# Kernel tuning notes

Hardware: AMD Instinct MI355X
Metric: run time of the kernel (lower is better)

The kernel has to match this reference:

```python
import jax, jax.numpy as jnp
import numpy as np

NUM_GROUPS = 8
EPS = 1e-5


def setup_inputs() -> dict:
    key = jax.random.key(0)
    ks = jax.random.split(key, 10)
    b, c, h, w = 4, 64, 64, 64
    x = jax.random.normal(ks[0], (b, c, h, w), dtype=jnp.float32)
    # GroupNorm affine params (default init: weight=1, bias=0; randomize slightly for testing)
    gamma = jnp.ones((c,), jnp.float32) + 0.01 * jax.random.normal(ks[1], (c,))
    beta = 0.01 * jax.random.normal(ks[2], (c,))
    # 1x1 conv weights as [out_c, in_c] matrices (xavier-uniform), biases zeros in torch init
    def xavier(k, shape):
        fan = shape[0] + shape[1]
        lim = jnp.sqrt(6.0 / fan)
        return jax.random.uniform(k, shape, jnp.float32, -lim, lim)
    Wq = xavier(ks[3], (c, c)); bq = jnp.zeros((c,), jnp.float32)
    Wk = xavier(ks[4], (c, c)); bk = jnp.zeros((c,), jnp.float32)
    Wv = xavier(ks[5], (c, c)); bv = jnp.zeros((c,), jnp.float32)
    Wp = xavier(ks[6], (c, c)); bp = jnp.zeros((c,), jnp.float32)
    return {"x": x, "gamma": gamma, "beta": beta,
            "Wq": Wq, "bq": bq, "Wk": Wk, "bk": bk,
            "Wv": Wv, "bv": bv, "Wp": Wp, "bp": bp}


def group_norm(x, gamma, beta):
    b, c, h, w = x.shape
    g = NUM_GROUPS
    xg = x.reshape(b, g, c // g, h, w)
    mean = jnp.mean(xg, axis=(2, 3, 4), keepdims=True)
    var = jnp.var(xg, axis=(2, 3, 4), keepdims=True)
    xn = ((xg - mean) * jax.lax.rsqrt(var + EPS)).reshape(b, c, h, w)
    return xn * gamma[None, :, None, None] + beta[None, :, None, None]


def reference(x, gamma, beta, Wq, bq, Wk, bk, Wv, bv, Wp, bp):
    b, c, h, w = x.shape
    n = h * w
    xn = group_norm(x, gamma, beta)
    xn_flat = xn.reshape(b, c, n)  # [b, c, n]
    # 1x1 convs == channel-wise linear maps
    q = jnp.einsum('oc,bcn->bno', Wq, xn_flat) + bq  # [b, n, c]
    k = jnp.einsum('oc,bcn->bon', Wk, xn_flat) + bk[None, :, None]  # [b, c, n]
    v = jnp.einsum('oc,bcn->bno', Wv, xn_flat) + bv  # [b, n, c]
    attn = jax.nn.softmax(jnp.einsum('bnc,bcm->bnm', q, k) / jnp.sqrt(jnp.float32(c)), axis=-1)
    out = jnp.einsum('bnm,bmc->bnc', attn, v)  # [b, n, c]
    out = out.transpose(0, 2, 1).reshape(b, c, h, w)
    out = jnp.einsum('oc,bchw->bohw', Wp, out) + bp[None, :, None, None]
    return out + x
```

## Files before the change

kernel.cpp:

```cpp
#include <hip/hip_runtime.h>
#include <hip/hip_bf16.h>
#include <math.h>

#define BATCH 4
#define CH    64
#define NPOS  4096
#define NGRP  8
#define CPG   8
#define GEPS  1e-5f
#define NSPLIT 8
#define LOG2E 1.4426950408889634f

typedef __attribute__((ext_vector_type(8))) short bf16x8;
typedef __attribute__((ext_vector_type(4))) float f32x4;

__device__ __forceinline__ ushort f2bf(float f) {
    union { float f; uint32_t u; } v; v.f = f;
    uint32_t r = v.u + 0x7fffu + ((v.u >> 16) & 1u);
    return (ushort)(r >> 16);
}
__device__ __forceinline__ float bf2f(ushort u) {
    union { uint32_t u; float f; } v; v.u = ((uint32_t)u) << 16; return v.f;
}

__device__ __forceinline__ uint32_t swz(uint32_t row, uint32_t byteInRow) {
    return (row << 7) + (byteInRow ^ ((row & 7u) << 4));
}

__device__ __forceinline__ bf16x8 ldfrag(const ushort* base, int row, int kbyte) {
    return *(const bf16x8*)((const char*)base + swz(row, kbyte));
}

__global__ __launch_bounds__(256) void gn_part_kernel(const float* __restrict__ x,
                                                      float2* __restrict__ part) {
    const int blk = blockIdx.x;
    const float4* xp4 = (const float4*)(x + (size_t)blk * 4096);
    float s1 = 0.f, s2 = 0.f;
    for (int i = threadIdx.x; i < 1024; i += 256) {
        float4 t = xp4[i];
        s1 += t.x + t.y + t.z + t.w;
        s2 += t.x * t.x + t.y * t.y + t.z * t.z + t.w * t.w;
    }
    __shared__ float sh1[256], sh2[256];
    const int tid = threadIdx.x;
    sh1[tid] = s1; sh2[tid] = s2;
    __syncthreads();
    for (int off = 128; off > 0; off >>= 1) {
        if (tid < off) { sh1[tid] += sh1[tid + off]; sh2[tid] += sh2[tid + off]; }
        __syncthreads();
    }
    if (tid == 0) { float2 r; r.x = sh1[0]; r.y = sh2[0]; part[blk] = r; }
}

__global__ __launch_bounds__(256) void qkv_mfma_kernel(
    const float* __restrict__ x, const float2* __restrict__ part,
    const float* __restrict__ gamma, const float* __restrict__ beta,
    const float* __restrict__ Wq, const float* __restrict__ bq,
    const float* __restrict__ Wk, const float* __restrict__ bk,
    const float* __restrict__ Wv, const float* __restrict__ bv,
    ushort* __restrict__ qg, ushort* __restrict__ kg, ushort* __restrict__ vg)
{
    __shared__ ushort xn[64 * 64];
    __shared__ ushort Wl[64 * 64];
    __shared__ ushort ob[64 * 64];
    __shared__ float st[16];

    const int tid = threadIdx.x;
    const int w = tid >> 6, lane = tid & 63, g = lane >> 4, q16 = lane & 15;
    const int m = blockIdx.x >> 8;
    const int bidx = blockIdx.x & 255;
    const int b = bidx >> 6, n0 = (bidx & 63) << 6;

    const float* W = (m == 0) ? Wq : (m == 1) ? Wk : Wv;

    {
        const int row = tid >> 2, cb = (tid & 3) << 4;
#pragma unroll
        for (int j = 0; j < 4; ++j) {
            float4 v = *(const float4*)(W + row * 64 + cb + j * 4);
            ushort4 h; h.x = f2bf(v.x); h.y = f2bf(v.y); h.z = f2bf(v.z); h.w = f2bf(v.w);
            *(ushort4*)((char*)Wl + swz(row, (cb + j * 4) * 2)) = h;
        }
    }
    if (tid < 64) {
        float2 p = part[b * 64 + tid];
        float s1 = p.x, s2 = p.y;
        s1 += __shfl_xor(s1, 1); s2 += __shfl_xor(s2, 1);
        s1 += __shfl_xor(s1, 2); s2 += __shfl_xor(s2, 2);
        s1 += __shfl_xor(s1, 4); s2 += __shfl_xor(s2, 4);
        if ((tid & 7) == 0) {
            const float inv = 1.0f / (float)(CPG * NPOS);
            float mean = s1 * inv;
            float var  = s2 * inv - mean * mean;
            st[(tid >> 3) * 2]     = mean;
            st[(tid >> 3) * 2 + 1] = rsqrtf(var + GEPS);
        }
    }
    __syncthreads();

    {
        const int c = tid >> 2, nb = (tid & 3) << 4;
        const float mean = st[(c >> 3) * 2];
        const float rstd = st[(c >> 3) * 2 + 1];
        const float gmm = gamma[c] * rstd;
        const float btt = beta[c] - mean * gmm;
        const float* xp = x + (((size_t)(b * CH + c)) << 12) + n0 + nb;
#pragma unroll
        for (int j = 0; j < 4; ++j) {
            float4 v = *(const float4*)(xp + j * 4);
            float vv[4] = {v.x, v.y, v.z, v.w};
#pragma unroll
            for (int e = 0; e < 4; ++e) {
                int n = nb + j * 4 + e;
                *(ushort*)((char*)xn + swz(n, c * 2)) = f2bf(vv[e] * gmm + btt);
            }
        }
    }
    __syncthreads();

    if (m < 2) {
        const float* bias = m ? bk : bq;
        const float scl = m ? 1.0f : 0.125f * LOG2E;
        bf16x8 ax0 = ldfrag(xn, (w << 4) + q16, (g << 4));
        bf16x8 ax1 = ldfrag(xn, (w << 4) + q16, 64 + (g << 4));
#pragma unroll
        for (int ot = 0; ot < 4; ++ot) {
            f32x4 acc = {0.f, 0.f, 0.f, 0.f};
            bf16x8 b0 = ldfrag(Wl, (ot << 4) + q16, (g << 4));
            bf16x8 b1 = ldfrag(Wl, (ot << 4) + q16, 64 + (g << 4));
            acc = __builtin_amdgcn_mfma_f32_16x16x32_bf16(ax0, b0, acc, 0, 0, 0);
            acc = __builtin_amdgcn_mfma_f32_16x16x32_bf16(ax1, b1, acc, 0, 0, 0);
            float bs = bias[(ot << 4) + q16];
#pragma unroll
            for (int r = 0; r < 4; ++r)
                *(ushort*)((char*)ob + swz((w << 4) + (g << 2) + r, ((ot << 4) + q16) << 1)) =
                    f2bf((acc[r] + bs) * scl);
        }
        __syncthreads();
        ushort* dst = (m ? kg : qg) + (((size_t)b) << 18);
#pragma unroll
        for (int i = 0; i < 2; ++i) {
            const int G = tid + (i << 8);
            const int lane_ = G & 63;
            const int h = (G >> 6) & 1;
            const int colb = (h << 5) + ((lane_ >> 4) << 3);
            if (m == 0) {
                const int qgi = (G >> 7) & 1;
                const int qgl = G >> 8;
                const int row = (qgl << 5) + (qgi << 4) + (lane_ & 15);
                int4 d = *(const int4*)((char*)ob + swz(row, colb << 1));
                *(int4*)(dst + (((size_t)(n0 >> 5) + qgl) << 11)
                             + ((size_t)((((qgi << 1) + h) << 6) + lane_) << 3)) = d;
            } else {
                const int nt = G >> 7;
                const int row = (nt << 4) + (lane_ & 15);
                int4 d = *(const int4*)((char*)ob + swz(row, colb << 1));
                *(int4*)(dst + ((size_t)(n0 >> 6) << 12)
                             + ((size_t)((((nt << 1) + h) << 6) + lane_) << 3)) = d;
            }
        }
    } else {
        bf16x8 aw0 = ldfrag(Wl, (w << 4) + q16, (g << 4));
        bf16x8 aw1 = ldfrag(Wl, (w << 4) + q16, 64 + (g << 4));
#pragma unroll
        for (int nt = 0; nt < 4; ++nt) {
            f32x4 acc = {0.f, 0.f, 0.f, 0.f};
            bf16x8 b0 = ldfrag(xn, (nt << 4) + q16, (g << 4));
            bf16x8 b1 = ldfrag(xn, (nt << 4) + q16, 64 + (g << 4));
            acc = __builtin_amdgcn_mfma_f32_16x16x32_bf16(aw0, b0, acc, 0, 0, 0);
            acc = __builtin_amdgcn_mfma_f32_16x16x32_bf16(aw1, b1, acc, 0, 0, 0);
#pragma unroll
            for (int r = 0; r < 4; ++r) {
                float bs = bv[(w << 4) + (g << 2) + r];
                *(ushort*)((char*)ob + swz((w << 4) + (g << 2) + r, ((nt << 4) + q16) << 1)) =
                    f2bf(acc[r] + bs);
            }
        }
        __syncthreads();
        ushort* dst = vg + (((size_t)b) << 18) + ((size_t)(n0 >> 6) << 12);
#pragma unroll
        for (int i = 0; i < 2; ++i) {
            const int G = tid + (i << 8);
            const int lane_ = G & 63;
            const int h = (G >> 6) & 1;
            const int ct = G >> 7;
            const int row = (ct << 4) + (lane_ & 15);
            const int colb = (h << 5) + ((lane_ >> 4) << 3);
            int4 d = *(const int4*)((char*)ob + swz(row, colb << 1));
            *(int4*)(dst + ((size_t)((((ct << 1) + h) << 6) + lane_) << 3)) = d;
        }
    }
}

#define LOADK(KF, KT)                                                          \
    _Pragma("unroll") for (int nt = 0; nt < 4; ++nt)                           \
    _Pragma("unroll") for (int h = 0; h < 2; ++h)                              \
        KF[nt][h] = *(const bf16x8*)(kp + (((size_t)(KT)) << 12) +             \
                     ((size_t)((((nt << 1) + h) << 6) + lane) << 3));

#define STEP(KF, KFN, KT, PREF)                                                \
  do {                                                                         \
    bf16x8 vf[4][2];                                                           \
    _Pragma("unroll") for (int ct = 0; ct < 4; ++ct)                           \
    _Pragma("unroll") for (int h = 0; h < 2; ++h)                              \
        vf[ct][h] = *(const bf16x8*)(vp + (((size_t)(KT)) << 12) +             \
                     ((size_t)((((ct << 1) + h) << 6) + lane) << 3));          \
    if (PREF) { LOADK(KFN, (KT) + 1); }                                        \
    f32x4 s_[4][2];                                                            \
    _Pragma("unroll") for (int nt = 0; nt < 4; ++nt)                           \
    _Pragma("unroll") for (int qgi = 0; qgi < 2; ++qgi) {                      \
        f32x4 z = {0.f, 0.f, 0.f, 0.f};                                        \
        z = __builtin_amdgcn_mfma_f32_16x16x32_bf16(KF[nt][0], aq[qgi][0], z, 0, 0, 0); \
        z = __builtin_amdgcn_mfma_f32_16x16x32_bf16(KF[nt][1], aq[qgi][1], z, 0, 0, 0); \
        s_[nt][qgi] = z;                                                       \
    }                                                                          \
    _Pragma("unroll") for (int qgi = 0; qgi < 2; ++qgi) {                      \
        float rs = 0.0f;                                                       \
        _Pragma("unroll") for (int nt = 0; nt < 4; ++nt) {                     \
            float p0 = exp2f(s_[nt][qgi][0]);                                  \
            float p1 = exp2f(s_[nt][qgi][1]);                                  \
            float p2 = exp2f(s_[nt][qgi][2]);                                  \
            float p3 = exp2f(s_[nt][qgi][3]);                                  \
            rs += (p0 + p1) + (p2 + p3);                                       \
            float2 t01; t01.x = p0; t01.y = p1;                                \
            float2 t23; t23.x = p2; t23.y = p3;                                \
            __hip_bfloat162 b01 = __float22bfloat162_rn(t01);                  \
            __hip_bfloat162 b23 = __float22bfloat162_rn(t23);                  \
            uint2 pk; pk.x = *(uint32_t*)&b01; pk.y = *(uint32_t*)&b23;        \
            *(uint2*)((char*)Pw + swz((qgi << 4) + q16, (nt << 5) + (lg << 3))) = pk; \
        }                                                                      \
        rs += __shfl_xor(rs, 16);                                              \
        rs += __shfl_xor(rs, 32);                                              \
        l_[qgi] += rs;                                                         \
    }                                                                          \
    asm volatile("" ::: "memory");                                             \
    bf16x8 pb[2][2];                                                           \
    _Pragma("unroll") for (int qgi = 0; qgi < 2; ++qgi) {                      \
        pb[qgi][0] = ldfrag(Pw, (qgi << 4) + q16, (lg << 4));                  \
        pb[qgi][1] = ldfrag(Pw, (qgi << 4) + q16, 64 + (lg << 4));             \
    }                                                                          \
    _Pragma("unroll") for (int ct = 0; ct < 4; ++ct)                           \
    _Pragma("unroll") for (int qgi = 0; qgi < 2; ++qgi) {                      \
        f32x4 o = o_[ct][qgi];                                                 \
        o = __builtin_amdgcn_mfma_f32_16x16x32_bf16(vf[ct][0], pb[qgi][0], o, 0, 0, 0); \
        o = __builtin_amdgcn_mfma_f32_16x16x32_bf16(vf[ct][1], pb[qgi][1], o, 0, 0, 0); \
        o_[ct][qgi] = o;                                                       \
    }                                                                          \
  } while (0)

__global__ __launch_bounds__(256) void attn_mfma_kernel(
    const ushort* __restrict__ qg, const ushort* __restrict__ kg,
    const ushort* __restrict__ vg,
    ushort* __restrict__ opart, float* __restrict__ lpart)
{
    __shared__ ushort Ps[4][32 * 64];

    const int tid = threadIdx.x;
    const int w = tid >> 6, lane = tid & 63, lg = lane >> 4, q16 = lane & 15;
    const int logical = ((blockIdx.x & 7) << 7) + (blockIdx.x >> 3);
    const int ks = logical & 7;
    const int qb = (logical >> 3) & 31;
    const int b  = logical >> 8;
    const int q0 = (qb << 7) + (w << 5);
    const ushort* qp = qg + (((size_t)b) << 18) + ((size_t)((qb << 2) + w) << 11);
    const ushort* kp = kg + (((size_t)b) << 18) + ((size_t)ks << 15);
    const ushort* vp = vg + (((size_t)b) << 18) + ((size_t)ks << 15);
    ushort* Pw = Ps[w];

    bf16x8 aq[2][2];
#pragma unroll
    for (int qgi = 0; qgi < 2; ++qgi)
#pragma unroll
        for (int h = 0; h < 2; ++h)
            aq[qgi][h] = *(const bf16x8*)(qp + ((size_t)((((qgi << 1) + h) << 6) + lane) << 3));

    float l_[2] = {0.f, 0.f};
    f32x4 o_[4][2];
#pragma unroll
    for (int ct = 0; ct < 4; ++ct)
#pragma unroll
        for (int qgi = 0; qgi < 2; ++qgi) o_[ct][qgi] = (f32x4){0.f, 0.f, 0.f, 0.f};

    bf16x8 kfA[4][2], kfB[4][2];
    LOADK(kfA, 0);

#pragma unroll 1
    for (int kt2 = 0; kt2 < 8; kt2 += 2) {
        STEP(kfA, kfB, kt2, true);
        STEP(kfB, kfA, kt2 + 1, (kt2 + 1) < 7);
    }

    const size_t bs = (size_t)(b * NSPLIT + ks);
#pragma unroll
    for (int qgi = 0; qgi < 2; ++qgi) {
        const int n = q0 + (qgi << 4) + q16;
        ushort* ob = opart + ((bs * 64) << 12) + n;
#pragma unroll
        for (int ct = 0; ct < 4; ++ct)
#pragma unroll
            for (int r = 0; r < 4; ++r)
                ob[((size_t)((ct << 4) + (lg << 2) + r)) << 12] = f2bf(o_[ct][qgi][r]);
    }
    if (lg == 0) {
#pragma unroll
        for (int qgi = 0; qgi < 2; ++qgi) {
            const int n = q0 + (qgi << 4) + q16;
            lpart[bs * 4096 + n] = l_[qgi];
        }
    }
}

__global__ __launch_bounds__(256) void combine_kernel(
    const ushort* __restrict__ opart, const float* __restrict__ lpart,
    const float* __restrict__ x, const float* __restrict__ Wp,
    const float* __restrict__ bp, float* __restrict__ out)
{
    __shared__ ushort Obf[64 * 64];
    __shared__ ushort Wps[64 * 64];
    __shared__ float as_[64];

    const int tid = threadIdx.x;
    const int w = tid >> 6, lane = tid & 63, g = lane >> 4, q16 = lane & 15;
    const int b = blockIdx.x >> 6, n0 = (blockIdx.x & 63) << 6;

    {
        const int row = tid >> 2, cb = (tid & 3) << 4;
#pragma unroll
        for (int j = 0; j < 4; ++j) {
            float4 v = *(const float4*)(Wp + row * 64 + cb + j * 4);
            ushort4 h; h.x = f2bf(v.x); h.y = f2bf(v.y); h.z = f2bf(v.z); h.w = f2bf(v.w);
            *(ushort4*)((char*)Wps + swz(row, (cb + j * 4) * 2)) = h;
        }
    }
    if (tid < 64) {
        const int n = n0 + tid;
        float d = 0.f;
#pragma unroll
        for (int s = 0; s < NSPLIT; ++s)
            d += lpart[(size_t)(b * NSPLIT + s) * 4096 + n];
        as_[tid] = 1.0f / d;
    }
    __syncthreads();

    {
        const int c = tid >> 2, nb = (tid & 3) << 4;
        const ushort* base = opart + ((((size_t)(b * NSPLIT)) * 64 + c) << 12) + n0 + nb;
        const size_t sstride = (size_t)64 << 12;
        float acc[16];
#pragma unroll
        for (int e = 0; e < 16; ++e) acc[e] = 0.f;
#pragma unroll
        for (int s = 0; s < NSPLIT; ++s) {
            const ushort* p = base + s * sstride;
            uint4 d0 = *(const uint4*)(p);
            uint4 d1 = *(const uint4*)(p + 8);
            const uint uw[8] = {d0.x, d0.y, d0.z, d0.w, d1.x, d1.y, d1.z, d1.w};
#pragma unroll
            for (int j = 0; j < 8; ++j) {
                acc[2 * j]     += bf2f((ushort)(uw[j] & 0xffffu));
                acc[2 * j + 1] += bf2f((ushort)(uw[j] >> 16));
            }
        }
#pragma unroll
        for (int e = 0; e < 16; ++e) {
            int nl = nb + e;
            *(ushort*)((char*)Obf + swz(nl, c << 1)) = f2bf(acc[e] * as_[nl]);
        }
    }
    __syncthreads();

    {
        bf16x8 aw0 = ldfrag(Wps, (w << 4) + q16, (g << 4));
        bf16x8 aw1 = ldfrag(Wps, (w << 4) + q16, 64 + (g << 4));
        float bpv[4];
#pragma unroll
        for (int r = 0; r < 4; ++r) bpv[r] = bp[(w << 4) + (g << 2) + r];
#pragma unroll
        for (int qt = 0; qt < 4; ++qt) {
            f32x4 d = {0.f, 0.f, 0.f, 0.f};
            bf16x8 b0 = ldfrag(Obf, (qt << 4) + q16, (g << 4));
            bf16x8 b1 = ldfrag(Obf, (qt << 4) + q16, 64 + (g << 4));
            d = __builtin_amdgcn_mfma_f32_16x16x32_bf16(aw0, b0, d, 0, 0, 0);
            d = __builtin_amdgcn_mfma_f32_16x16x32_bf16(aw1, b1, d, 0, 0, 0);
#pragma unroll
            for (int r = 0; r < 4; ++r) {
                int oc = (w << 4) + (g << 2) + r;
                size_t addr = (((size_t)(b * CH + oc)) << 12) + n0 + (qt << 4) + q16;
                out[addr] = d[r] + bpv[r] + x[addr];
            }
        }
    }
}

extern "C" void kernel_launch(void* const* d_in, const int* in_sizes, int n_in,
                              void* d_out, int out_size, void* d_ws, size_t ws_size,
                              hipStream_t stream) {
    const float* x     = (const float*)d_in[0];
    const float* gamma = (const float*)d_in[1];
    const float* beta  = (const float*)d_in[2];
    const float* Wq    = (const float*)d_in[3];
    const float* bq    = (const float*)d_in[4];
    const float* Wk    = (const float*)d_in[5];
    const float* bk    = (const float*)d_in[6];
    const float* Wv    = (const float*)d_in[7];
    const float* bv    = (const float*)d_in[8];
    const float* Wp    = (const float*)d_in[9];
    const float* bp    = (const float*)d_in[10];
    float* out = (float*)d_out;

    float2* part = (float2*)d_ws;
    ushort* q_t = (ushort*)((char*)d_ws + 4096);
    ushort* k_t = q_t + (size_t)BATCH * NPOS * CH;
    ushort* v_t = k_t + (size_t)BATCH * NPOS * CH;
    ushort* opart = (ushort*)((char*)d_ws + 4096 + (size_t)3 * BATCH * NPOS * CH * 2);
    float* lpart = (float*)((char*)opart + (size_t)BATCH * NSPLIT * CH * NPOS * 2);

    hipLaunchKernelGGL(gn_part_kernel, dim3(256), dim3(256), 0, stream, x, part);
    hipLaunchKernelGGL(qkv_mfma_kernel, dim3(768), dim3(256), 0, stream,
                       x, part, gamma, beta, Wq, bq, Wk, bk, Wv, bv, q_t, k_t, v_t);
    hipLaunchKernelGGL(attn_mfma_kernel, dim3(1024), dim3(256), 0, stream,
                       q_t, k_t, v_t, opart, lpart);
    hipLaunchKernelGGL(combine_kernel, dim3(BATCH * 64), dim3(256), 0, stream,
                       opart, lpart, x, Wp, bp, out);
}
```

Baseline: 53.68 us.

## Process 64 queries per wave in attention kernel to reuse K/V fragments

Each wave in the attention kernel now handles 64 query rows instead of 32, so each K and V tile loaded from global memory feeds twice as many MFMAs. The grid shrinks from 1024 to 512 blocks and the shared P scratch doubles. The explicit double-buffered K prefetch macro is dropped in favour of loading K per n-tile inside the loop. This cuts K/V global traffic per query, at the cost of more registers (accumulators double), lower occupancy, fewer blocks for 256 CUs, and less latency hiding for K loads.

Result: slower. 63.46 us (+18.2%).

```diff
diff --git a/kernel.cpp b/kernel.cpp
--- a/kernel.cpp
+++ b/kernel.cpp
@@ -192,107 +192,110 @@
     }
 }
 
-#define LOADK(KF, KT)                                                          \
-    _Pragma("unroll") for (int nt = 0; nt < 4; ++nt)                           \
-    _Pragma("unroll") for (int h = 0; h < 2; ++h)                              \
-        KF[nt][h] = *(const bf16x8*)(kp + (((size_t)(KT)) << 12) +             \
-                     ((size_t)((((nt << 1) + h) << 6) + lane) << 3));
-
-#define STEP(KF, KFN, KT, PREF)                                                \
-  do {                                                                         \
-    bf16x8 vf[4][2];                                                           \
-    _Pragma("unroll") for (int ct = 0; ct < 4; ++ct)                           \
-    _Pragma("unroll") for (int h = 0; h < 2; ++h)                              \
-        vf[ct][h] = *(const bf16x8*)(vp + (((size_t)(KT)) << 12) +             \
-                     ((size_t)((((ct << 1) + h) << 6) + lane) << 3));          \
-    if (PREF) { LOADK(KFN, (KT) + 1); }                                        \
-    f32x4 s_[4][2];                                                            \
-    _Pragma("unroll") for (int nt = 0; nt < 4; ++nt)                           \
-    _Pragma("unroll") for (int qgi = 0; qgi < 2; ++qgi) {                      \
-        f32x4 z = {0.f, 0.f, 0.f, 0.f};                                        \
-        z = __builtin_amdgcn_mfma_f32_16x16x32_bf16(KF[nt][0], aq[qgi][0], z, 0, 0, 0); \
-        z = __builtin_amdgcn_mfma_f32_16x16x32_bf16(KF[nt][1], aq[qgi][1], z, 0, 0, 0); \
-        s_[nt][qgi] = z;                                                       \
-    }                                                                          \
-    _Pragma("unroll") for (int qgi = 0; qgi < 2; ++qgi) {                      \
-        float rs = 0.0f;                                                       \
-        _Pragma("unroll") for (int nt = 0; nt < 4; ++nt) {                     \
-            float p0 = exp2f(s_[nt][qgi][0]);                                  \
-            float p1 = exp2f(s_[nt][qgi][1]);                                  \
-            float p2 = exp2f(s_[nt][qgi][2]);                                  \
-            float p3 = exp2f(s_[nt][qgi][3]);                                  \
-            rs += (p0 + p1) + (p2 + p3);                                       \
-            float2 t01; t01.x = p0; t01.y = p1;                                \
-            float2 t23; t23.x = p2; t23.y = p3;                                \
-            __hip_bfloat162 b01 = __float22bfloat162_rn(t01);                  \
-            __hip_bfloat162 b23 = __float22bfloat162_rn(t23);                  \
-            uint2 pk; pk.x = *(uint32_t*)&b01; pk.y = *(uint32_t*)&b23;        \
-            *(uint2*)((char*)Pw + swz((qgi << 4) + q16, (nt << 5) + (lg << 3))) = pk; \
-        }                                                                      \
-        rs += __shfl_xor(rs, 16);                                              \
-        rs += __shfl_xor(rs, 32);                                              \
-        l_[qgi] += rs;                                                         \
-    }                                                                          \
-    asm volatile("" ::: "memory");                                             \
-    bf16x8 pb[2][2];                                                           \
-    _Pragma("unroll") for (int qgi = 0; qgi < 2; ++qgi) {                      \
-        pb[qgi][0] = ldfrag(Pw, (qgi << 4) + q16, (lg << 4));                  \
-        pb[qgi][1] = ldfrag(Pw, (qgi << 4) + q16, 64 + (lg << 4));             \
-    }                                                                          \
-    _Pragma("unroll") for (int ct = 0; ct < 4; ++ct)                           \
-    _Pragma("unroll") for (int qgi = 0; qgi < 2; ++qgi) {                      \
-        f32x4 o = o_[ct][qgi];                                                 \
-        o = __builtin_amdgcn_mfma_f32_16x16x32_bf16(vf[ct][0], pb[qgi][0], o, 0, 0, 0); \
-        o = __builtin_amdgcn_mfma_f32_16x16x32_bf16(vf[ct][1], pb[qgi][1], o, 0, 0, 0); \
-        o_[ct][qgi] = o;                                                       \
-    }                                                                          \
-  } while (0)
-
 __global__ __launch_bounds__(256) void attn_mfma_kernel(
     const ushort* __restrict__ qg, const ushort* __restrict__ kg,
     const ushort* __restrict__ vg,
     ushort* __restrict__ opart, float* __restrict__ lpart)
 {
-    __shared__ ushort Ps[4][32 * 64];
+    __shared__ ushort Ps[4][64 * 64];
 
     const int tid = threadIdx.x;
     const int w = tid >> 6, lane = tid & 63, lg = lane >> 4, q16 = lane & 15;
-    const int logical = ((blockIdx.x & 7) << 7) + (blockIdx.x >> 3);
+    const int logical = ((blockIdx.x & 7) << 6) + (blockIdx.x >> 3);
     const int ks = logical & 7;
-    const int qb = (logical >> 3) & 31;
-    const int b  = logical >> 8;
-    const int q0 = (qb << 7) + (w << 5);
-    const ushort* qp = qg + (((size_t)b) << 18) + ((size_t)((qb << 2) + w) << 11);
+    const int qb = (logical >> 3) & 15;
+    const int b  = logical >> 7;
+    const int q0 = (qb << 8) + (w << 6);
+    const int qw64 = (qb << 2) + w;
+
+    const ushort* qp = qg + (((size_t)b) << 18);
     const ushort* kp = kg + (((size_t)b) << 18) + ((size_t)ks << 15);
     const ushort* vp = vg + (((size_t)b) << 18) + ((size_t)ks << 15);
     ushort* Pw = Ps[w];
 
-    bf16x8 aq[2][2];
-#pragma unroll
-    for (int qgi = 0; qgi < 2; ++qgi)
+    bf16x8 aq[4][2];
+#pragma unroll
+    for (int qgi = 0; qgi < 4; ++qgi)
 #pragma unroll
         for (int h = 0; h < 2; ++h)
-            aq[qgi][h] = *(const bf16x8*)(qp + ((size_t)((((qgi << 1) + h) << 6) + lane) << 3));
-
-    float l_[2] = {0.f, 0.f};
-    f32x4 o_[4][2];
+            aq[qgi][h] = *(const bf16x8*)(qp
+                + ((size_t)((qw64 << 1) + (qgi >> 1)) << 11)
+                + ((size_t)(((((qgi & 1) << 1) + h) << 6) + lane) << 3));
+
+    float l_[4] = {0.f, 0.f, 0.f, 0.f};
+    f32x4 o_[4][4];
 #pragma unroll
     for (int ct = 0; ct < 4; ++ct)
 #pragma unroll
-        for (int qgi = 0; qgi < 2; ++qgi) o_[ct][qgi] = (f32x4){0.f, 0.f, 0.f, 0.f};
-
-    bf16x8 kfA[4][2], kfB[4][2];
-    LOADK(kfA, 0);
+        for (int qgi = 0; qgi < 4; ++qgi) o_[ct][qgi] = (f32x4){0.f, 0.f, 0.f, 0.f};
 
 #pragma unroll 1
-    for (int kt2 = 0; kt2 < 8; kt2 += 2) {
-        STEP(kfA, kfB, kt2, true);
-        STEP(kfB, kfA, kt2 + 1, (kt2 + 1) < 7);
+    for (int kt = 0; kt < 8; ++kt) {
+        bf16x8 vf[4][2];
+#pragma unroll
+        for (int ct = 0; ct < 4; ++ct)
+#pragma unroll
+            for (int h = 0; h < 2; ++h)
+                vf[ct][h] = *(const bf16x8*)(vp + (((size_t)kt) << 12) +
+                             ((size_t)((((ct << 1) + h) << 6) + lane) << 3));
+        float rs[4] = {0.f, 0.f, 0.f, 0.f};
+#pragma unroll
+        for (int nt = 0; nt < 4; ++nt) {
+            bf16x8 k0 = *(const bf16x8*)(kp + (((size_t)kt) << 12) +
+                         ((size_t)(((nt << 1) << 6) + lane) << 3));
+            bf16x8 k1 = *(const bf16x8*)(kp + (((size_t)kt) << 12) +
+                         ((size_t)((((nt << 1) + 1) << 6) + lane) << 3));
+            f32x4 s[4];
+#pragma unroll
+            for (int qgi = 0; qgi < 4; ++qgi) {
+                f32x4 z = {0.f, 0.f, 0.f, 0.f};
+                z = __builtin_amdgcn_mfma_f32_16x16x32_bf16(k0, aq[qgi][0], z, 0, 0, 0);
+                z = __builtin_amdgcn_mfma_f32_16x16x32_bf16(k1, aq[qgi][1], z, 0, 0, 0);
+                s[qgi] = z;
+            }
+#pragma unroll
+            for (int qgi = 0; qgi < 4; ++qgi) {
+                float p0 = exp2f(s[qgi][0]);
+                float p1 = exp2f(s[qgi][1]);
+                float p2 = exp2f(s[qgi][2]);
+                float p3 = exp2f(s[qgi][3]);
+                rs[qgi] += (p0 + p1) + (p2 + p3);
+                float2 t01; t01.x = p0; t01.y = p1;
+                float2 t23; t23.x = p2; t23.y = p3;
+                __hip_bfloat162 b01 = __float22bfloat162_rn(t01);
+                __hip_bfloat162 b23 = __float22bfloat162_rn(t23);
+                uint2 pk; pk.x = *(uint32_t*)&b01; pk.y = *(uint32_t*)&b23;
+                *(uint2*)((char*)Pw + swz((qgi << 4) + q16, (nt << 5) + (lg << 3))) = pk;
+            }
+        }
+#pragma unroll
+        for (int qgi = 0; qgi < 4; ++qgi) {
+            float r = rs[qgi];
+            r += __shfl_xor(r, 16);
+            r += __shfl_xor(r, 32);
+            l_[qgi] += r;
+        }
+        asm volatile("" ::: "memory");
+        bf16x8 pb[4][2];
+#pragma unroll
+        for (int qgi = 0; qgi < 4; ++qgi) {
+            pb[qgi][0] = ldfrag(Pw, (qgi << 4) + q16, (lg << 4));
+            pb[qgi][1] = ldfrag(Pw, (qgi << 4) + q16, 64 + (lg << 4));
+        }
+#pragma unroll
+        for (int ct = 0; ct < 4; ++ct)
+#pragma unroll
+            for (int qgi = 0; qgi < 4; ++qgi) {
+                f32x4 o = o_[ct][qgi];
+                o = __builtin_amdgcn_mfma_f32_16x16x32_bf16(vf[ct][0], pb[qgi][0], o, 0, 0, 0);
+                o = __builtin_amdgcn_mfma_f32_16x16x32_bf16(vf[ct][1], pb[qgi][1], o, 0, 0, 0);
+                o_[ct][qgi] = o;
+            }
     }
 
     const size_t bs = (size_t)(b * NSPLIT + ks);
 #pragma unroll
-    for (int qgi = 0; qgi < 2; ++qgi) {
+    for (int qgi = 0; qgi < 4; ++qgi) {
         const int n = q0 + (qgi << 4) + q16;
         ushort* ob = opart + ((bs * 64) << 12) + n;
 #pragma unroll
@@ -303,7 +306,7 @@
     }
     if (lg == 0) {
 #pragma unroll
-        for (int qgi = 0; qgi < 2; ++qgi) {
+        for (int qgi = 0; qgi < 4; ++qgi) {
             const int n = q0 + (qgi << 4) + q16;
             lpart[bs * 4096 + n] = l_[qgi];
         }
@@ -418,7 +421,7 @@
     hipLaunchKernelGGL(gn_part_kernel, dim3(256), dim3(256), 0, stream, x, part);
     hipLaunchKernelGGL(qkv_mfma_kernel, dim3(768), dim3(256), 0, stream,
                        x, part, gamma, beta, Wq, bq, Wk, bk, Wv, bv, q_t, k_t, v_t);
-    hipLaunchKernelGGL(attn_mfma_kernel, dim3(1024), dim3(256), 0, stream,
+    hipLaunchKernelGGL(attn_mfma_kernel, dim3(512), dim3(256), 0, stream,
                        q_t, k_t, v_t, opart, lpart);
     hipLaunchKernelGGL(combine_kernel, dim3(BATCH * 64), dim3(256), 0, stream,
                        opart, lpart, x, Wp, bp, out);
```

## Software-pipeline attention: overlap QK^T/exp of next tile with PV of current

Applied to the files above, without the earlier changes.

Splits the per-tile step into a score/exp block and a PV block, then double-buffers the P tile in shared memory so the scores of tile t+1 are computed before the PV MMA of tile t. The row-sum shuffles move out of the loop and run once at the end. It also adds a launch-bounds occupancy hint of 4 blocks. The aim is to hide exp and LDS latency behind MFMA work, at the cost of twice the shared memory per wave and higher register pressure.

New measurement: 76.07 us. +41.7%, slower.

```diff
diff --git a/kernel.cpp b/kernel.cpp
--- a/kernel.cpp
+++ b/kernel.cpp
@@ -198,14 +198,8 @@
         KF[nt][h] = *(const bf16x8*)(kp + (((size_t)(KT)) << 12) +             \
                      ((size_t)((((nt << 1) + h) << 6) + lane) << 3));
 
-#define STEP(KF, KFN, KT, PREF)                                                \
+#define SBLOCK(KF, PA)                                                         \
   do {                                                                         \
-    bf16x8 vf[4][2];                                                           \
-    _Pragma("unroll") for (int ct = 0; ct < 4; ++ct)                           \
-    _Pragma("unroll") for (int h = 0; h < 2; ++h)                              \
-        vf[ct][h] = *(const bf16x8*)(vp + (((size_t)(KT)) << 12) +             \
-                     ((size_t)((((ct << 1) + h) << 6) + lane) << 3));          \
-    if (PREF) { LOADK(KFN, (KT) + 1); }                                        \
     f32x4 s_[4][2];                                                            \
     _Pragma("unroll") for (int nt = 0; nt < 4; ++nt)                           \
     _Pragma("unroll") for (int qgi = 0; qgi < 2; ++qgi) {                      \
@@ -215,29 +209,33 @@
         s_[nt][qgi] = z;                                                       \
     }                                                                          \
     _Pragma("unroll") for (int qgi = 0; qgi < 2; ++qgi) {                      \
-        float rs = 0.0f;                                                       \
         _Pragma("unroll") for (int nt = 0; nt < 4; ++nt) {                     \
             float p0 = exp2f(s_[nt][qgi][0]);                                  \
             float p1 = exp2f(s_[nt][qgi][1]);                                  \
             float p2 = exp2f(s_[nt][qgi][2]);                                  \
             float p3 = exp2f(s_[nt][qgi][3]);                                  \
-            rs += (p0 + p1) + (p2 + p3);                                       \
+            l_[qgi] += (p0 + p1) + (p2 + p3);                                  \
             float2 t01; t01.x = p0; t01.y = p1;                                \
             float2 t23; t23.x = p2; t23.y = p3;                                \
             __hip_bfloat162 b01 = __float22bfloat162_rn(t01);                  \
             __hip_bfloat162 b23 = __float22bfloat162_rn(t23);                  \
             uint2 pk; pk.x = *(uint32_t*)&b01; pk.y = *(uint32_t*)&b23;        \
-            *(uint2*)((char*)Pw + swz((qgi << 4) + q16, (nt << 5) + (lg << 3))) = pk; \
+            *(uint2*)((char*)(PA) + swz((qgi << 4) + q16, (nt << 5) + (lg << 3))) = pk; \
         }                                                                      \
-        rs += __shfl_xor(rs, 16);                                              \
-        rs += __shfl_xor(rs, 32);                                              \
-        l_[qgi] += rs;                                                         \
     }                                                                          \
-    asm volatile("" ::: "memory");                                             \
+  } while (0)
+
+#define PVBLOCK(PA, KT)                                                        \
+  do {                                                                         \
+    bf16x8 vf[4][2];                                                           \
+    _Pragma("unroll") for (int ct = 0; ct < 4; ++ct)                           \
+    _Pragma("unroll") for (int h = 0; h < 2; ++h)                              \
+        vf[ct][h] = *(const bf16x8*)(vp + (((size_t)(KT)) << 12) +             \
+                     ((size_t)((((ct << 1) + h) << 6) + lane) << 3));          \
     bf16x8 pb[2][2];                                                           \
     _Pragma("unroll") for (int qgi = 0; qgi < 2; ++qgi) {                      \
-        pb[qgi][0] = ldfrag(Pw, (qgi << 4) + q16, (lg << 4));                  \
-        pb[qgi][1] = ldfrag(Pw, (qgi << 4) + q16, 64 + (lg << 4));             \
+        pb[qgi][0] = ldfrag((PA), (qgi << 4) + q16, (lg << 4));                \
+        pb[qgi][1] = ldfrag((PA), (qgi << 4) + q16, 64 + (lg << 4));           \
     }                                                                          \
     _Pragma("unroll") for (int ct = 0; ct < 4; ++ct)                           \
     _Pragma("unroll") for (int qgi = 0; qgi < 2; ++qgi) {                      \
@@ -248,12 +246,12 @@
     }                                                                          \
   } while (0)
 
-__global__ __launch_bounds__(256) void attn_mfma_kernel(
+__global__ __launch_bounds__(256, 4) void attn_mfma_kernel(
     const ushort* __restrict__ qg, const ushort* __restrict__ kg,
     const ushort* __restrict__ vg,
     ushort* __restrict__ opart, float* __restrict__ lpart)
 {
-    __shared__ ushort Ps[4][32 * 64];
+    __shared__ ushort Ps[4][2][32 * 64];
 
     const int tid = threadIdx.x;
     const int w = tid >> 6, lane = tid & 63, lg = lane >> 4, q16 = lane & 15;
@@ -265,7 +263,8 @@
     const ushort* qp = qg + (((size_t)b) << 18) + ((size_t)((qb << 2) + w) << 11);
     const ushort* kp = kg + (((size_t)b) << 18) + ((size_t)ks << 15);
     const ushort* vp = vg + (((size_t)b) << 18) + ((size_t)ks << 15);
-    ushort* Pw = Ps[w];
+    ushort* P0 = Ps[w][0];
+    ushort* P1 = Ps[w][1];
 
     bf16x8 aq[2][2];
 #pragma unroll
@@ -283,11 +282,26 @@
 
     bf16x8 kfA[4][2], kfB[4][2];
     LOADK(kfA, 0);
+    LOADK(kfB, 1);
+    SBLOCK(kfA, P0);
 
 #pragma unroll 1
-    for (int kt2 = 0; kt2 < 8; kt2 += 2) {
-        STEP(kfA, kfB, kt2, true);
-        STEP(kfB, kfA, kt2 + 1, (kt2 + 1) < 7);
+    for (int t = 0; t < 6; t += 2) {
+        LOADK(kfA, t + 2);
+        SBLOCK(kfB, P1);
+        PVBLOCK(P0, t);
+        LOADK(kfB, t + 3);
+        SBLOCK(kfA, P0);
+        PVBLOCK(P1, t + 1);
+    }
+    SBLOCK(kfB, P1);
+    PVBLOCK(P0, 6);
+    PVBLOCK(P1, 7);
+
+#pragma unroll
+    for (int qgi = 0; qgi < 2; ++qgi) {
+        l_[qgi] += __shfl_xor(l_[qgi], 16);
+        l_[qgi] += __shfl_xor(l_[qgi], 32);
     }
 
     const size_t bs = (size_t)(b * NSPLIT + ks);
```
